# Optimization experiments

Measured on AMD Instinct MI355X. Metric: run time of the kernel, lower is better.

## Reference

```python
import jax, jax.numpy as jnp
import numpy as np

DIM = 16      # latent_dim == sec
SEC = 16
SUB = 16      # sub_sec
E = SEC * SUB # num_elements = 256
TH = 0.2
BATCH = 128
SL = BATCH // 2
TAU = 0.0001

bexpm = jax.vmap(jax.scipy.linalg.expm)


def _commut(ge):
    # commutative(div=dim): loop over K=E//DIM block pairs with cumulative block
    # swaps; loss = sum_k cumsum(per-pair sq-diff)[k] / (DIM*E)^2
    K = E // DIM
    basis = ge.reshape(DIM, DIM * E)                 # [d, d*E]
    bm = jnp.matmul(ge, basis).reshape(DIM * E, DIM * E)
    R = bm[:K * DIM, :K * DIM].reshape(K, DIM, K, DIM)
    c = 2.0 * ((R - jnp.transpose(R, (2, 1, 0, 3))) ** 2).sum((1, 3))  # [K,K]
    iu, ju = np.triu_indices(K, k=1)                 # lexicographic pair order
    return jnp.cumsum(c[iu, ju]).sum() / float((DIM * E) ** 2)


def _independent(z, ge, sec_idx):
    B = z.shape[0]
    syms = bexpm(ge)                                 # [E,d,d]
    diff = z - jnp.matmul(z, syms)                   # [E,B,d]
    d2 = (diff ** 2).reshape(-1, DIM)
    sparse = jnp.mean((d2.sum(-1) - d2.max(-1)) ** 2)
    par = diff.reshape(SEC, SUB * B, DIM)            # [SEC,M,d]
    nrm = jnp.linalg.norm(par, axis=-1, keepdims=True)
    nn_ = jnp.einsum('smi,sni->smn', nrm, nrm)       # [SEC,M,M]
    dd = jnp.einsum('smd,snd->smn', par, par)
    parallel = jnp.mean(-jnp.log((dd / nn_) ** 2 + 1e-9))
    sel = diff.reshape(SEC, SUB, B, DIM)[jnp.arange(SEC), sec_idx]
    sel = sel.reshape(SEC * B, DIM)
    sn = jnp.linalg.norm(sel, axis=-1, keepdims=True)
    ratio = (sel @ sel.T) / (sn @ sn.T)
    mask = jnp.asarray(1.0 - np.kron(np.eye(SEC, dtype=np.float32),
                                     np.ones((B, B), np.float32)))
    orth = jnp.mean((ratio ** 2) * mask)
    return orth, parallel, _commut(ge), sparse


def reference(mean, logvar, latent_z, group_elements, lin_w, lin_b,
              gumbel_noise, sec_idx):
    B = latent_z.shape[0]
    sl = B // 2
    mean1, mean2 = mean[:sl], mean[sl:]
    std1 = jnp.exp(0.5 * logvar[:sl])
    std2 = jnp.exp(0.5 * mean[sl:])   # (faithful to source bug: uses mean)
    z1, z2 = latent_z[:sl], latent_z[sl:]
    orth, parallel, commut, sparse = _independent(latent_z, group_elements, sec_idx)

    zd = z1 - z2
    target = (jnp.abs(zd) > TH).astype(jnp.int32).reshape(-1)   # [sl*SEC]
    feat = jnp.concatenate([mean1, std1, mean2, std2], -1)       # [sl,4d]
    prob = feat @ lin_w.T + lin_b                                # [sl,18*SEC]
    sector_logits = prob[:, :2 * SEC].reshape(-1, 2)             # [sl*SEC,2]
    p = jax.nn.softmax(sector_logits, -1)
    ls = jax.nn.log_softmax(p, -1)    # cross_entropy applied to softmax output
    sector_loss = -jnp.take_along_axis(ls, target[:, None], 1).sum() / sl

    attn = jax.nn.softmax((sector_logits + gumbel_noise) / TAU, -1)
    switch = jnp.where((attn[:, 0] >= 0.5) | (attn[:, 1] > 0.5), attn[:, 1], 0.0)
    switch = switch.reshape(sl, SEC)
    fprob = jax.nn.softmax(prob[:, 2 * SEC:].reshape(sl, SEC, SUB), -1)
    fprob = fprob.reshape(sl, E)
    w = jnp.repeat(switch, SUB, axis=-1) * fprob                 # [sl,E]
    syms = w[:, :, None, None] * group_elements[None]            # [sl,E,d,d]
    sub_syms = syms.reshape(sl, SEC, SUB, DIM, DIM).sum(2)       # [sl,SEC,d,d]
    S = syms.sum(1)                                              # [sl,d,d]
    fwd_syms = bexpm(S)
    inv_syms = bexpm(-S)
    attn_score = jnp.concatenate([switch, fprob], -1)            # [sl,SEC+E]

    tz1 = jnp.einsum('bd,bde->be', z1, fwd_syms)
    tz2 = jnp.einsum('bd,bde->be', z2, inv_syms)
    equivariant = jnp.mean((tz2 - z1) ** 2) + jnp.mean((tz1 - z2) ** 2)
    return (tz1, tz2, fwd_syms, equivariant, attn_score,
            orth, parallel, commut, sparse, sector_loss, sub_syms)


def setup_inputs() -> dict:
    key = jax.random.key(0)
    ks = jax.random.split(key, 7)
    mean = jax.random.normal(ks[0], (BATCH, DIM), jnp.float32)
    logvar = jax.random.normal(ks[1], (BATCH, DIM), jnp.float32)
    latent_z = jax.random.normal(ks[2], (BATCH, DIM), jnp.float32)
    group_elements = 0.1 * jax.random.normal(ks[3], (E, DIM, DIM), jnp.float32)
    lin_w = 0.1 * jax.random.normal(ks[4], ((SUB + 2) * SEC, 4 * DIM), jnp.float32)
    lin_b = jnp.zeros(((SUB + 2) * SEC,), jnp.float32)
    u = jax.random.uniform(ks[5], (SL * SEC, 2), jnp.float32, 1e-6, 1.0 - 1e-6)
    gumbel_noise = -jnp.log(-jnp.log(u))
    sec_idx = jax.random.randint(ks[6], (SEC,), 0, SEC, jnp.int32)
    return {'mean': mean, 'logvar': logvar, 'latent_z': latent_z,
            'group_elements': group_elements, 'lin_w': lin_w, 'lin_b': lin_b,
            'gumbel_noise': gumbel_noise, 'sec_idx': sec_idx}
```

## Files before the change

### kernel.cpp

```cpp
#include <hip/hip_runtime.h>
#include <math.h>

#define O_TZ1      0
#define O_TZ2      1024
#define O_FWD      2048
#define O_EQUI     18432
#define O_ATTN     18433
#define O_ORTH     35841
#define O_PAR      35842
#define O_COMM     35843
#define O_SPARSE   35844
#define O_SECLOSS  35845
#define O_SUB      35846

#define P_SECLOSS  0
#define P_SPARSE   64
#define P_CPAIR    320
#define P_EQUI     440
#define P_PAR      504
#define P_ORTH     2680

typedef short s16x8 __attribute__((ext_vector_type(8)));
typedef float f32x4 __attribute__((ext_vector_type(4)));

__device__ __forceinline__ void block_store(float v, float* red, int t, float* slot, float scale)
{
    red[t] = v;
    __syncthreads();
    for (int off = 128; off > 0; off >>= 1) { if (t < off) red[t] += red[t+off]; __syncthreads(); }
    if (t == 0) *slot = red[0] * scale;
}

__device__ __forceinline__ void block_store2(float v, float* red4, int t, float* slot, float scale)
{
    #pragma unroll
    for (int off = 32; off > 0; off >>= 1) v += __shfl_down(v, off);
    if ((t & 63) == 0) red4[t >> 6] = v;
    __syncthreads();
    if (t == 0) *slot = (red4[0] + red4[1] + red4[2] + red4[3]) * scale;
}

__device__ __forceinline__ unsigned short f2bf(float x)
{
    unsigned int u = __float_as_uint(x);
    u = (u + 0x7FFFu + ((u >> 16) & 1u)) >> 16;
    return (unsigned short)u;
}

__device__ __forceinline__ void expm_core(const float* __restrict__ src, float sign,
                                          float* sm, int* shi, int t)
{
    float* As = sm; float* T = sm + 256; float* P = sm + 512; float* rowsum = sm + 768;
    float a = src[t];
    As[t] = a;
    __syncthreads();
    if (t < 16) {
        float rs = 0.f;
        #pragma unroll
        for (int k = 0; k < 16; ++k) rs += fabsf(As[t*16+k]);
        rowsum[t] = rs;
    }
    __syncthreads();
    if (t == 0) {
        float nrm = 0.f;
        for (int i = 0; i < 16; ++i) nrm = fmaxf(nrm, rowsum[i]);
        int s = 0;
        if (nrm > 0.66f) { s = (int)ceilf(log2f(nrm * 1.51515f)); if (s < 0) s = 0; }
        *shi = s;
    }
    __syncthreads();
    int sq = *shi;
    float scale = sign * exp2f((float)(-sq));
    int i = t >> 4, j = t & 15;
    float as = a * scale;
    As[t] = as;
    T[t]  = ((i==j) ? 1.0f : 0.0f) + as;
    P[t]  = as;
    __syncthreads();
    for (int k = 2; k <= 8; ++k) {
        float accv = 0.f;
        #pragma unroll
        for (int m = 0; m < 16; ++m) accv += P[i*16+m]*As[m*16+j];
        float rk = 1.0f/(float)k;
        __syncthreads();
        float term = accv * rk;
        P[t] = term;
        T[t] += term;
        __syncthreads();
    }
    for (int q = 0; q < sq; ++q) {
        float accv = 0.f;
        #pragma unroll
        for (int m = 0; m < 16; ++m) accv += T[i*16+m]*T[m*16+j];
        __syncthreads();
        T[t] = accv;
        __syncthreads();
    }
}

template <bool DO_LOG>
__device__ __forceinline__ float gram_tile_lds(const unsigned short* __restrict__ diffb,
                                               short* tiles, int baseM, int baseN, int t)
{
    const uint4* gd = (const uint4*)diffb;
    #pragma unroll
    for (int q = 0; q < 2; ++q) {
        int idx = t + 256*q;
        int row = idx >> 1, half = idx & 1;
        int grow = (row < 128) ? (baseM + row) : (baseN + (row - 128));
        uint4 v = gd[grow*2 + half];
        *(uint4*)(tiles + row*24 + half*8) = v;
    }
    __syncthreads();
    int lane = t & 63, wave = t >> 6, quad = lane >> 4, col = lane & 15;
    s16x8 zf = {0,0,0,0,0,0,0,0};
    s16x8 A0=zf, A1=zf, B0=zf, B1=zf, B2=zf, B3=zf, B4=zf, B5=zf, B6=zf, B7=zf;
    if (quad < 2) {
        const short* tm_ = tiles;
        const short* tn_ = tiles + 128*24;
        A0 = *(const s16x8*)(tm_ + (wave*32      + col)*24 + quad*8);
        A1 = *(const s16x8*)(tm_ + (wave*32 + 16 + col)*24 + quad*8);
        B0 = *(const s16x8*)(tn_ + (  0 + col)*24 + quad*8);
        B1 = *(const s16x8*)(tn_ + ( 16 + col)*24 + quad*8);
        B2 = *(const s16x8*)(tn_ + ( 32 + col)*24 + quad*8);
        B3 = *(const s16x8*)(tn_ + ( 48 + col)*24 + quad*8);
        B4 = *(const s16x8*)(tn_ + ( 64 + col)*24 + quad*8);
        B5 = *(const s16x8*)(tn_ + ( 80 + col)*24 + quad*8);
        B6 = *(const s16x8*)(tn_ + ( 96 + col)*24 + quad*8);
        B7 = *(const s16x8*)(tn_ + (112 + col)*24 + quad*8);
    }
    f32x4 cz = {0.f, 0.f, 0.f, 0.f};
    float accf = 0.f;
#define GTILE(AF, BF) { \
    f32x4 c = __builtin_amdgcn_mfma_f32_16x16x32_bf16(AF, BF, cz, 0, 0, 0); \
    if (DO_LOG) { \
        float p0 = (c[0]*c[0] + 1e-9f) * (c[1]*c[1] + 1e-9f); \
        float p1 = (c[2]*c[2] + 1e-9f) * (c[3]*c[3] + 1e-9f); \
        accf += __log2f(p0 * p1); \
    } else { \
        accf += c[0]*c[0] + c[1]*c[1] + c[2]*c[2] + c[3]*c[3]; \
    } }
    GTILE(A0,B0) GTILE(A0,B1) GTILE(A0,B2) GTILE(A0,B3)
    GTILE(A0,B4) GTILE(A0,B5) GTILE(A0,B6) GTILE(A0,B7)
    GTILE(A1,B0) GTILE(A1,B1) GTILE(A1,B2) GTILE(A1,B3)
    GTILE(A1,B4) GTILE(A1,B5) GTILE(A1,B6) GTILE(A1,B7)
#undef GTILE
    return accf;
}

__global__ void k_stage1(const float* __restrict__ mean, const float* __restrict__ logvar,
                         const float* __restrict__ latent, const float* __restrict__ ge,
                         const float* __restrict__ lin_w, const float* __restrict__ lin_b,
                         const float* __restrict__ gumbel,
                         float* __restrict__ out, float* __restrict__ S_ws,
                         unsigned short* __restrict__ diffb, float* __restrict__ part)
{
    __shared__ float smem[4864];
    __shared__ int shi;
    int bid = blockIdx.x;
    int t = threadIdx.x;

    if (bid < 64) {
        int b = bid;
        float* feat = smem;
        float* probb = smem + 64;
        float* red16 = smem + 352;
        float* wrow = smem + 368;
        if (t < 64) {
            int k = t; float v;
            if (k < 16)       v = mean[b*16 + k];
            else if (k < 32)  v = expf(0.5f * logvar[b*16 + (k-16)]);
            else if (k < 48)  v = mean[(64+b)*16 + (k-32)];
            else              v = expf(0.5f * mean[(64+b)*16 + (k-48)]);
            feat[k] = v;
        }
        __syncthreads();
        for (int j = t; j < 288; j += 256) {
            float a = lin_b[j];
            const float* wr = lin_w + j*64;
            #pragma unroll
            for (int k = 0; k < 64; ++k) a += feat[k]*wr[k];
            probb[j] = a;
        }
        __syncthreads();
        if (t < 16) {
            int s = t;
            float l0 = probb[2*s], l1 = probb[2*s+1];
            float M = fmaxf(l0,l1);
            float e0 = expf(l0-M), e1 = expf(l1-M);
            float Z = e0+e1;
            float p0 = e0/Z, p1 = e1/Z;
            float M2 = fmaxf(p0,p1);
            float lse = M2 + logf(expf(p0-M2)+expf(p1-M2));
            float ls0 = p0 - lse, ls1 = p1 - lse;
            float z1v = latent[b*16+s], z2v = latent[(64+b)*16+s];
            int tt = (fabsf(z1v - z2v) > 0.2f) ? 1 : 0;
            red16[s] = -(tt ? ls1 : ls0);
            int r = b*16 + s;
            float x0 = (l0 + gumbel[2*r])   * 10000.0f;
            float x1 = (l1 + gumbel[2*r+1]) * 10000.0f;
            float Ma = fmaxf(x0,x1);
            float a0 = expf(x0-Ma), a1 = expf(x1-Ma);
            float Za = a0+a1;
            a0 /= Za; a1 /= Za;
            float sw = ((a0 >= 0.5f) || (a1 > 0.5f)) ? a1 : 0.0f;
            out[O_ATTN + b*272 + s] = sw;
            const float* fl = &probb[32 + s*16];
            float mf = fl[0];
            #pragma unroll
            for (int u = 1; u < 16; ++u) mf = fmaxf(mf, fl[u]);
            float ex[16]; float Zf = 0.f;
            #pragma unroll
            for (int u = 0; u < 16; ++u) { ex[u] = expf(fl[u]-mf); Zf += ex[u]; }
            float rZ = 1.0f/Zf;
            #pragma unroll
            for (int u = 0; u < 16; ++u) {
                float fp = ex[u]*rZ;
                out[O_ATTN + b*272 + 16 + s*16 + u] = fp;
                wrow[s*16 + u] = sw*fp;
            }
        }
        __syncthreads();
        if (t == 0) {
            float s = 0.f;
            for (int i = 0; i < 16; ++i) s += red16[i];
            part[P_SECLOSS + b] = s;
        }
        float Stot = 0.f;
        for (int s = 0; s < 16; ++s) {
            float a = 0.f;
            #pragma unroll
            for (int u = 0; u < 16; ++u)
                a += wrow[s*16+u] * ge[(s*16+u)*256 + t];
            out[O_SUB + b*4096 + s*256 + t] = a;
            Stot += a;
        }
        S_ws[b*256 + t] = Stot;
    } else if (bid < 320) {
        int e = bid - 64;
        float* zsh = smem + 784;
        float* red = smem + 2832;
        #pragma unroll
        for (int q = 0; q < 8; ++q) zsh[t+256*q] = latent[t+256*q];
        expm_core(ge + e*256, 1.0f, smem, &shi, t);
        const float* T = smem + 256;
        float pv = 0.f;
        if (t < 128) {
            float zr[16];
            #pragma unroll
            for (int k = 0; k < 16; ++k) zr[k] = zsh[t*16+k];
            float dv[16];
            float sum = 0.f, mx = 0.f;
            #pragma unroll
            for (int d = 0; d < 16; ++d) {
                float a = 0.f;
                #pragma unroll
                for (int k = 0; k < 16; ++k) a += zr[k]*T[k*16+d];
                float v = zr[d] - a;
                dv[d] = v;
                float v2 = v*v;
                sum += v2; mx = fmaxf(mx, v2);
            }
            float sm2 = sum - mx;
            pv = sm2*sm2;
            float ri = 1.0f / sqrtf(sum);
            unsigned int pk[8];
            #pragma unroll
            for (int d = 0; d < 8; ++d) {
                unsigned short h0 = f2bf(dv[2*d]   * ri);
                unsigned short h1 = f2bf(dv[2*d+1] * ri);
                pk[d] = (unsigned int)h0 | ((unsigned int)h1 << 16);
            }
            uint4* dst = (uint4*)(diffb + (size_t)(e*128 + t)*16);
            dst[0] = make_uint4(pk[0], pk[1], pk[2], pk[3]);
            dst[1] = make_uint4(pk[4], pk[5], pk[6], pk[7]);
        }
        block_store(pv, red, t, part + P_SPARSE + e, 1.0f);
    } else {
        int idx = bid - 320;
        float* G = smem;
        float* gA = smem + 4096;
        float* gB = smem + 4352;
        float* red = smem + 4608;
        int a2 = 0, cnt = 15, rem = idx;
        while (rem >= cnt) { rem -= cnt; a2++; cnt--; }
        int b2 = a2 + 1 + rem;
        #pragma unroll
        for (int q = 0; q < 16; ++q) {
            int ii = t + 256*q;
            int k = ii >> 8, x = ii & 255;
            G[ii] = ge[k*16*256 + x];
        }
        gA[t] = ge[a2*256+t];
        gB[t] = ge[b2*256+t];
        __syncthreads();
        int i = t >> 4, j = t & 15;
        float v1 = 0.f, v2 = 0.f;
        #pragma unroll
        for (int k = 0; k < 16; ++k) {
            v1 += gA[i*16+k]*G[k*256 + b2*16 + j];
            v2 += gB[i*16+k]*G[k*256 + a2*16 + j];
        }
        float d = v1 - v2;
        block_store(d*d, red, t, part + P_CPAIR + idx, 2.0f);
    }
}

__global__ void __launch_bounds__(256) k_stage2(const float* __restrict__ latent,
                                                const float* __restrict__ S_ws,
                                                const unsigned short* __restrict__ diffb,
                                                const int* __restrict__ sec_idx,
                                                float* __restrict__ out,
                                                float* __restrict__ part)
{
    __shared__ float smem[3328];
    __shared__ int shi;
    int bid = blockIdx.x;
    int t = threadIdx.x;
    float* red4 = smem + 3072;

    if (bid < 64) {
        int b = bid;
        expm_core(S_ws + b*256, 1.0f, smem, &shi, t);
        const float* T = smem + 256;
        out[O_FWD + b*256 + t] = T[t];
        float t1 = 0.f, z1d = 0.f, z2d = 0.f;
        if (t < 16) {
            int d = t;
            #pragma unroll
            for (int k = 0; k < 16; ++k) t1 += latent[b*16+k] * T[k*16+d];
            out[O_TZ1 + b*16 + d] = t1;
            z1d = latent[b*16+d];
            z2d = latent[(64+b)*16+d];
        }
        expm_core(S_ws + b*256, -1.0f, smem, &shi, t);
        float t2 = 0.f, ep = 0.f;
        if (t < 16) {
            int d = t;
            #pragma unroll
            for (int k = 0; k < 16; ++k) t2 += latent[(64+b)*16+k] * T[k*16+d];
            out[O_TZ2 + b*16 + d] = t2;
            ep = (t2 - z1d)*(t2 - z1d) + (t1 - z2d)*(t1 - z2d);
        }
        block_store2(ep, red4, t, part + P_EQUI + b, 1.0f);
    } else if (bid < 2240) {
        int tile = bid - 64;
        int s = tile & 15;
        int r = tile >> 4;
        int tm = 0;
        while (r >= 16 - tm) { r -= 16 - tm; tm++; }
        int tn = tm + r;
        float accf = gram_tile_lds<true>(diffb, (short*)smem, s*2048 + tm*128, s*2048 + tn*128, t);
        float wt = (tm == tn) ? 1.0f : 2.0f;
        block_store2(accf, red4, t, part + P_PAR + tile, wt);
    } else {
        int idx = bid - 2240;
        int sm = 0, cnt = 15, rem = idx;
        while (rem >= cnt) { rem -= cnt; sm++; cnt--; }
        int sn = sm + 1 + rem;
        int em = sm*16 + sec_idx[sm];
        int en = sn*16 + sec_idx[sn];
        float accf = gram_tile_lds<false>(diffb, (short*)smem, em*128, en*128, t);
        block_store2(accf, red4, t, part + P_ORTH + idx, 2.0f);
    }
}

__global__ void k_final(const float* __restrict__ part, float* __restrict__ out)
{
    __shared__ double dred[256];
    int t = threadIdx.x;

    double local = 0.0;
    for (int i = t; i < 2176; i += 256) local += (double)part[P_PAR + i];
    dred[t] = local;
    __syncthreads();
    for (int off = 128; off > 0; off >>= 1) { if (t < off) dred[t] += dred[t+off]; __syncthreads(); }
    double s_par = dred[0];
    __syncthreads();

    local = 0.0;
    if (t < 120) local += (double)part[P_ORTH + t];
    dred[t] = local;
    __syncthreads();
    for (int off = 128; off > 0; off >>= 1) { if (t < off) dred[t] += dred[t+off]; __syncthreads(); }
    double s_orth = dred[0];
    __syncthreads();

    local = 0.0;
    if (t < 64) local += (double)part[P_EQUI + t];
    dred[t] = local;
    __syncthreads();
    for (int off = 128; off > 0; off >>= 1) { if (t < off) dred[t] += dred[t+off]; __syncthreads(); }
    double s_equi = dred[0];
    __syncthreads();

    local = (t < 64) ? (double)part[P_SECLOSS + t] : 0.0;
    dred[t] = local;
    __syncthreads();
    for (int off = 128; off > 0; off >>= 1) { if (t < off) dred[t] += dred[t+off]; __syncthreads(); }
    double s_sec = dred[0];
    __syncthreads();

    dred[t] = (double)part[P_SPARSE + t];
    __syncthreads();
    for (int off = 128; off > 0; off >>= 1) { if (t < off) dred[t] += dred[t+off]; __syncthreads(); }
    double s_spa = dred[0];
    __syncthreads();

    local = 0.0;
    if (t < 120) local = (double)(120 - t) * (double)part[P_CPAIR + t];
    dred[t] = local;
    __syncthreads();
    for (int off = 128; off > 0; off >>= 1) { if (t < off) dred[t] += dred[t+off]; __syncthreads(); }

    if (t == 0) {
        out[O_COMM]    = (float)(dred[0] / 16777216.0);
        out[O_EQUI]    = (float)(s_equi / 1024.0);
        out[O_ORTH]    = (float)(s_orth / (2048.0*2048.0));
        out[O_PAR]     = (float)(-s_par * 0.6931471805599453 / 67108864.0);
        out[O_SPARSE]  = (float)(s_spa / 32768.0);
        out[O_SECLOSS] = (float)(s_sec / 64.0);
    }
}

extern "C" void kernel_launch(void* const* d_in, const int* in_sizes, int n_in,
                              void* d_out, int out_size, void* d_ws, size_t ws_size,
                              hipStream_t stream)
{
    const float* mean    = (const float*)d_in[0];
    const float* logvar  = (const float*)d_in[1];
    const float* latent  = (const float*)d_in[2];
    const float* ge      = (const float*)d_in[3];
    const float* lin_w   = (const float*)d_in[4];
    const float* lin_b   = (const float*)d_in[5];
    const float* gumbel  = (const float*)d_in[6];
    const int*   sec_idx = (const int*)d_in[7];
    float* out = (float*)d_out;

    char* ws = (char*)d_ws;
    float* part = (float*)ws;
    float* S_ws = (float*)(ws + 16384);
    unsigned short* diffb = (unsigned short*)(ws + 81920);

    k_stage1<<<440,  256, 0, stream>>>(mean, logvar, latent, ge, lin_w, lin_b, gumbel,
                                       out, S_ws, diffb, part);
    k_stage2<<<2360, 256, 0, stream>>>(latent, S_ws, diffb, sec_idx, out, part);
    k_final <<<1,    256, 0, stream>>>(part, out);
}
```

Before: 92.98 us.

## Fuse per-batch expm and equivariance work into stage1 blocks via LDS

The per-sample symmetry matrix S is now kept in shared memory, and the forward and inverse matrix exponentials, transformed latents and equivariance partials are computed inside the first-stage blocks. The second kernel is left with only the gram tiles. This removes the global round trip for S and 64 blocks from the second launch, and lets the expm work overlap with the other stage1 blocks. In exchange the first 64 stage1 blocks get longer, which could lengthen that kernel's critical path.

```diff
diff --git a/kernel.cpp b/kernel.cpp
--- a/kernel.cpp
+++ b/kernel.cpp
@@ -152,8 +152,8 @@
                          const float* __restrict__ latent, const float* __restrict__ ge,
                          const float* __restrict__ lin_w, const float* __restrict__ lin_b,
                          const float* __restrict__ gumbel,
-                         float* __restrict__ out, float* __restrict__ S_ws,
-                         unsigned short* __restrict__ diffb, float* __restrict__ part)
+                         float* __restrict__ out, unsigned short* __restrict__ diffb,
+                         float* __restrict__ part)
 {
     __shared__ float smem[4864];
     __shared__ int shi;
@@ -162,10 +162,12 @@
 
     if (bid < 64) {
         int b = bid;
-        float* feat = smem;
-        float* probb = smem + 64;
-        float* red16 = smem + 352;
-        float* wrow = smem + 368;
+        float* S_lds = smem + 784;
+        float* feat  = smem + 1040;
+        float* probb = smem + 1104;
+        float* red16 = smem + 1392;
+        float* wrow  = smem + 1408;
+        float* red   = smem + 1664;
         if (t < 64) {
             int k = t; float v;
             if (k < 16)       v = mean[b*16 + k];
@@ -235,7 +237,32 @@
             out[O_SUB + b*4096 + s*256 + t] = a;
             Stot += a;
         }
-        S_ws[b*256 + t] = Stot;
+        S_lds[t] = Stot;
+        __syncthreads();
+        expm_core(S_lds, 1.0f, smem, &shi, t);
+        const float* T = smem + 256;
+        out[O_FWD + b*256 + t] = T[t];
+        float t1 = 0.f, z1d = 0.f, z2d = 0.f;
+        if (t < 16) {
+            int d = t;
+            #pragma unroll
+            for (int k = 0; k < 16; ++k) t1 += latent[b*16+k] * T[k*16+d];
+            out[O_TZ1 + b*16 + d] = t1;
+            z1d = latent[b*16+d];
+            z2d = latent[(64+b)*16+d];
+        }
+        __syncthreads();
+        expm_core(S_lds, -1.0f, smem, &shi, t);
+        float t2 = 0.f, ep = 0.f;
+        if (t < 16) {
+            int d = t;
+            #pragma unroll
+            for (int k = 0; k < 16; ++k) t2 += latent[(64+b)*16+k] * T[k*16+d];
+            out[O_TZ2 + b*16 + d] = t2;
+            ep = (t2 - z1d)*(t2 - z1d) + (t1 - z2d)*(t1 - z2d);
+        }
+        __syncthreads();
+        block_store(ep, red, t, part + P_EQUI + b, 1.0f);
     } else if (bid < 320) {
         int e = bid - 64;
         float* zsh = smem + 784;
@@ -306,55 +333,26 @@
     }
 }
 
-__global__ void __launch_bounds__(256) k_stage2(const float* __restrict__ latent,
-                                                const float* __restrict__ S_ws,
-                                                const unsigned short* __restrict__ diffb,
+__global__ void __launch_bounds__(256) k_stage2(const unsigned short* __restrict__ diffb,
                                                 const int* __restrict__ sec_idx,
-                                                float* __restrict__ out,
                                                 float* __restrict__ part)
 {
-    __shared__ float smem[3328];
-    __shared__ int shi;
+    __shared__ float smem[3076];
     int bid = blockIdx.x;
     int t = threadIdx.x;
     float* red4 = smem + 3072;
 
-    if (bid < 64) {
-        int b = bid;
-        expm_core(S_ws + b*256, 1.0f, smem, &shi, t);
-        const float* T = smem + 256;
-        out[O_FWD + b*256 + t] = T[t];
-        float t1 = 0.f, z1d = 0.f, z2d = 0.f;
-        if (t < 16) {
-            int d = t;
-            #pragma unroll
-            for (int k = 0; k < 16; ++k) t1 += latent[b*16+k] * T[k*16+d];
-            out[O_TZ1 + b*16 + d] = t1;
-            z1d = latent[b*16+d];
-            z2d = latent[(64+b)*16+d];
-        }
-        expm_core(S_ws + b*256, -1.0f, smem, &shi, t);
-        float t2 = 0.f, ep = 0.f;
-        if (t < 16) {
-            int d = t;
-            #pragma unroll
-            for (int k = 0; k < 16; ++k) t2 += latent[(64+b)*16+k] * T[k*16+d];
-            out[O_TZ2 + b*16 + d] = t2;
-            ep = (t2 - z1d)*(t2 - z1d) + (t1 - z2d)*(t1 - z2d);
-        }
-        block_store2(ep, red4, t, part + P_EQUI + b, 1.0f);
-    } else if (bid < 2240) {
-        int tile = bid - 64;
-        int s = tile & 15;
-        int r = tile >> 4;
+    if (bid < 2176) {
+        int s = bid & 15;
+        int r = bid >> 4;
         int tm = 0;
         while (r >= 16 - tm) { r -= 16 - tm; tm++; }
         int tn = tm + r;
         float accf = gram_tile_lds<true>(diffb, (short*)smem, s*2048 + tm*128, s*2048 + tn*128, t);
         float wt = (tm == tn) ? 1.0f : 2.0f;
-        block_store2(accf, red4, t, part + P_PAR + tile, wt);
+        block_store2(accf, red4, t, part + P_PAR + bid, wt);
     } else {
-        int idx = bid - 2240;
+        int idx = bid - 2176;
         int sm = 0, cnt = 15, rem = idx;
         while (rem >= cnt) { rem -= cnt; sm++; cnt--; }
         int sn = sm + 1 + rem;
@@ -439,11 +437,10 @@
 
     char* ws = (char*)d_ws;
     float* part = (float*)ws;
-    float* S_ws = (float*)(ws + 16384);
-    unsigned short* diffb = (unsigned short*)(ws + 81920);
+    unsigned short* diffb = (unsigned short*)(ws + 16384);
 
     k_stage1<<<440,  256, 0, stream>>>(mean, logvar, latent, ge, lin_w, lin_b, gumbel,
-                                       out, S_ws, diffb, part);
-    k_stage2<<<2360, 256, 0, stream>>>(latent, S_ws, diffb, sec_idx, out, part);
+                                       out, diffb, part);
+    k_stage2<<<2296, 256, 0, stream>>>(diffb, sec_idx, part);
     k_final <<<1,    256, 0, stream>>>(part, out);
 }
```

Measured after the change: 96.83 us. 1.04x slower.
